# Performance work log

Hardware: AMD Instinct MI355X
Metric: run time of the kernel (lower is better)

## Reference

```python
import jax, jax.numpy as jnp
import numpy as np

B, N, M, E, CD, H, DH, MH = 4, 2048, 512, 512, 256, 8, 64, 1024
EPS = 1e-6

def _ln(x):
    m = x.mean(-1, keepdims=True)
    v = ((x - m) ** 2).mean(-1, keepdims=True)
    return (x - m) / jnp.sqrt(v + EPS)

def _heads(t):  # [B, L, H*DH] -> [B, H, L, DH]
    b, l, _ = t.shape
    return t.reshape(b, l, H, DH).transpose(0, 2, 1, 3)

def _attn(q, k, v, scale):
    sim = jnp.einsum('bhid,bhjd->bhij', q, k) * scale
    a = jax.nn.softmax(sim, axis=-1)
    o = jnp.einsum('bhij,bhjd->bhid', a, v)
    b, h, l, d = o.shape
    return o.transpose(0, 2, 1, 3).reshape(b, l, h * d)

def setup_inputs() -> dict:
    key = jax.random.key(0)
    ks = jax.random.split(key, 16)
    s = 0.02
    return {
        'cond': jax.random.normal(ks[0], (B, M, CD), jnp.float32),
        'x_in': jax.random.normal(ks[1], (B, N, E), jnp.float32),
        # nn.MultiheadAttention params (combined in-proj + out-proj)
        'Wqkv': jax.random.normal(ks[2], (3 * E, E), jnp.float32) * s,
        'b_qkv': jnp.zeros((3 * E,), jnp.float32),
        'Wo': jax.random.normal(ks[3], (E, E), jnp.float32) * s,
        'bo': jnp.zeros((E,), jnp.float32),
        # CrossAttention params (q/k/v no bias, out has bias)
        'Wcq': jax.random.normal(ks[4], (H * DH, E), jnp.float32) * s,
        'Wck': jax.random.normal(ks[5], (H * DH, CD), jnp.float32) * s,
        'Wcv': jax.random.normal(ks[6], (H * DH, CD), jnp.float32) * s,
        'Wco': jax.random.normal(ks[7], (E, H * DH), jnp.float32) * s,
        'bco': jnp.zeros((E,), jnp.float32),
        # MLP params (note: ReLU applied after the LAST layer too, per source)
        'W1': jax.random.normal(ks[8], (MH, E), jnp.float32) * s,
        'b1': jnp.zeros((MH,), jnp.float32),
        'W2': jax.random.normal(ks[9], (E, MH), jnp.float32) * s,
        'b2': jnp.zeros((E,), jnp.float32),
    }

def reference(cond, x_in, Wqkv, b_qkv, Wo, bo, Wcq, Wck, Wcv, Wco, bco, W1, b1, W2, b2):
    # --- self-attention (nn.MultiheadAttention math) ---
    xn = _ln(x_in)
    qkv = xn @ Wqkv.T + b_qkv  # [B,N,3E]
    q, k, v = jnp.split(qkv, 3, axis=-1)
    sa = _attn(_heads(q), _heads(k), _heads(v), 1.0 / jnp.sqrt(jnp.float32(DH)))
    x = sa @ Wo.T + bo + x_in
    # --- cross-attention ---
    xn2 = _ln(x)
    cq = _heads(xn2 @ Wcq.T)
    ck = _heads(cond @ Wck.T)
    cv = _heads(cond @ Wcv.T)
    ca = _attn(cq, ck, cv, DH ** -0.5)
    x = ca @ Wco.T + bco + x
    # --- MLP (ReLU after both layers, as in source) ---
    xn3 = _ln(x)
    h = jax.nn.relu(xn3 @ W1.T + b1)
    m = jax.nn.relu(h @ W2.T + b2)
    return m + x
```

## Files before the change

kernel.cpp:

```cpp
#include <hip/hip_runtime.h>
#include <cstdint>
#include <cstddef>


typedef short short8 __attribute__((ext_vector_type(8)));
typedef short short4v __attribute__((ext_vector_type(4)));
typedef float f32x4 __attribute__((ext_vector_type(4)));
typedef float f32x16 __attribute__((ext_vector_type(16)));

typedef __attribute__((address_space(1))) const void gconst_t;
typedef __attribute__((address_space(3))) void lds_t;

__device__ __forceinline__ void gl_lds16(const void* g, void* l) {
  __builtin_amdgcn_global_load_lds((gconst_t*)g, (lds_t*)l, 16, 0, 0);
}

__device__ __forceinline__ short f2bf(float f) {
  union { float f; unsigned u; } x; x.f = f;
  unsigned r = x.u + 0x7fffu + ((x.u >> 16) & 1u);
  return (short)(r >> 16);
}
__device__ __forceinline__ float bf2f(short s) {
  union { unsigned u; float f; } x; x.u = ((unsigned)(unsigned short)s) << 16;
  return x.f;
}

__device__ __forceinline__ void pl32swap(unsigned& a, unsigned& b) {
  asm("v_permlane32_swap_b32 %0, %1" : "+v"(a), "+v"(b));
}

struct CastDesc { const float* src; short* dst; int nblk; };
struct CastArgs { CastDesc d[9]; };

__global__ __launch_bounds__(256) void cast_multi(CastArgs a) {
  int bi = blockIdx.x;
#pragma unroll
  for (int i = 0; i < 9; ++i) {
    if (bi < a.d[i].nblk) {
      int idx = (bi * 256 + threadIdx.x) * 8;
      const float* src = a.d[i].src;
      float4 f0 = *(const float4*)(src + idx);
      float4 f1 = *(const float4*)(src + idx + 4);
      short8 o;
      o[0] = f2bf(f0.x); o[1] = f2bf(f0.y); o[2] = f2bf(f0.z); o[3] = f2bf(f0.w);
      o[4] = f2bf(f1.x); o[5] = f2bf(f1.y); o[6] = f2bf(f1.z); o[7] = f2bf(f1.w);
      *(short8*)(a.d[i].dst + idx) = o;
      return;
    }
    bi -= a.d[i].nblk;
  }
}

template <bool INBF>
__global__ __launch_bounds__(256) void ln_kernel(
    const void* __restrict__ xin, short* __restrict__ out, int nrows) {
  int row = blockIdx.x * 4 + (threadIdx.x >> 6);
  int lane = threadIdx.x & 63;
  if (row >= nrows) return;
  float v[8];
  if constexpr (INBF) {
    const short* xr = (const short*)xin + (size_t)row * 512 + lane * 8;
    short8 a = *(const short8*)xr;
#pragma unroll
    for (int e = 0; e < 8; ++e) v[e] = bf2f(a[e]);
  } else {
    const float* xr = (const float*)xin + (size_t)row * 512 + lane * 8;
    float4 a = *(const float4*)xr;
    float4 b = *(const float4*)(xr + 4);
    v[0] = a.x; v[1] = a.y; v[2] = a.z; v[3] = a.w;
    v[4] = b.x; v[5] = b.y; v[6] = b.z; v[7] = b.w;
  }
  float s = 0.f;
#pragma unroll
  for (int e = 0; e < 8; ++e) s += v[e];
#pragma unroll
  for (int m = 1; m < 64; m <<= 1) s += __shfl_xor(s, m);
  float mean = s * (1.f / 512.f);
  float sq = 0.f;
#pragma unroll
  for (int e = 0; e < 8; ++e) { float d = v[e] - mean; sq += d * d; }
#pragma unroll
  for (int m = 1; m < 64; m <<= 1) sq += __shfl_xor(sq, m);
  float rstd = rsqrtf(sq * (1.f / 512.f) + 1e-6f);
  short8 o;
#pragma unroll
  for (int e = 0; e < 8; ++e) o[e] = f2bf((v[e] - mean) * rstd);
  *(short8*)(out + (size_t)row * 512 + lane * 8) = o;
}

template <int TN, int RESMODE, bool BIAS, bool RELU, bool OUTBF, bool VT>
__global__ __launch_bounds__(256) void gemm_nt(
    const short* __restrict__ A, const short* __restrict__ W,
    const float* __restrict__ bias, const void* __restrict__ res,
    void* __restrict__ outp, int R, int NC, int K, int gx,
    short* __restrict__ vt, int vcol0, int vn_log2,
    float oscale, int oscale_end) {
  constexpr int NF = TN / 32;
  constexpr int NBUF = (TN == 128) ? 2 : 3;
  __shared__ short As[NBUF][128 * 64];
  __shared__ short Ws[NBUF][TN * 64];
  const int nwg = gridDim.x;
  const int b0 = blockIdx.x;
  const int bid = ((nwg & 7) == 0) ? ((b0 & 7) * (nwg >> 3) + (b0 >> 3)) : b0;
  const int bx = bid % gx, by = bid / gx;
  const int brow = by * 128, bcol = bx * TN;
  const int t = threadIdx.x;
  const int wid = t >> 6, lane = t & 63;
  const int lr = lane & 15, lk = lane >> 4;
  const int wrow = (wid >> 1) * 64, wcol = (wid & 1) * (TN / 2);
  f32x4 acc[4][NF] = {};

  const int srw = lane >> 3;
  const int scol = (((lane & 7) ^ srw) << 3);
  const short* Ag = A + (size_t)(brow + wid * 32 + srw) * K + scol;
  const short* Wg = W + (size_t)(bcol + wid * (TN / 4) + srw) * K + scol;

#define G_STAGE(I, BUF)                                                       \
  {                                                                           \
    const int k0_ = (I) * 64;                                                 \
    gl_lds16(Ag + k0_, &As[BUF][(wid * 32) * 64]);                            \
    gl_lds16(Ag + (size_t)8 * K + k0_, &As[BUF][(wid * 32 + 8) * 64]);        \
    gl_lds16(Ag + (size_t)16 * K + k0_, &As[BUF][(wid * 32 + 16) * 64]);      \
    gl_lds16(Ag + (size_t)24 * K + k0_, &As[BUF][(wid * 32 + 24) * 64]);      \
    if constexpr (TN == 128) {                                                \
      gl_lds16(Wg + k0_, &Ws[BUF][(wid * 32) * 64]);                          \
      gl_lds16(Wg + (size_t)8 * K + k0_, &Ws[BUF][(wid * 32 + 8) * 64]);      \
      gl_lds16(Wg + (size_t)16 * K + k0_, &Ws[BUF][(wid * 32 + 16) * 64]);    \
      gl_lds16(Wg + (size_t)24 * K + k0_, &Ws[BUF][(wid * 32 + 24) * 64]);    \
    } else {                                                                  \
      gl_lds16(Wg + k0_, &Ws[BUF][(wid * 16) * 64]);                          \
      gl_lds16(Wg + (size_t)8 * K + k0_, &Ws[BUF][(wid * 16 + 8) * 64]);      \
    }                                                                         \
  }

  const int ns = K / 64;

#define G_COMPUTE(CUR)                                                        \
  {                                                                           \
    _Pragma("unroll")                                                         \
    for (int kc = 0; kc < 2; ++kc) {                                          \
      short8 af[4], bf[NF];                                                   \
      _Pragma("unroll")                                                       \
      for (int mi = 0; mi < 4; ++mi) {                                        \
        const int row = wrow + mi * 16 + lr;                                  \
        af[mi] = *(const short8*)&As[CUR][row * 64 +                          \
                                          (((kc * 4 + lk) ^ (row & 7)) << 3)];\
      }                                                                       \
      _Pragma("unroll")                                                       \
      for (int ni = 0; ni < NF; ++ni) {                                       \
        const int row = wcol + ni * 16 + lr;                                  \
        bf[ni] = *(const short8*)&Ws[CUR][row * 64 +                          \
                                          (((kc * 4 + lk) ^ (row & 7)) << 3)];\
      }                                                                       \
      _Pragma("unroll")                                                       \
      for (int mi = 0; mi < 4; ++mi)                                          \
        _Pragma("unroll")                                                     \
        for (int ni = 0; ni < NF; ++ni)                                       \
          acc[mi][ni] = __builtin_amdgcn_mfma_f32_16x16x32_bf16(              \
              af[mi], bf[ni], acc[mi][ni], 0, 0, 0);                          \
    }                                                                         \
  }

  if constexpr (TN == 128) {
    G_STAGE(0, 0);
    asm volatile("s_waitcnt vmcnt(0)" ::: "memory");
    __builtin_amdgcn_s_barrier();
    for (int i = 0; i < ns; ++i) {
      const int cur = i & 1;
      if (i + 1 < ns) G_STAGE(i + 1, cur ^ 1);
      G_COMPUTE(cur);
      if (i + 1 < ns) {
        asm volatile("s_waitcnt vmcnt(0) lgkmcnt(0)" ::: "memory");
        __builtin_amdgcn_s_barrier();
      }
    }
  } else {
    G_STAGE(0, 0);
    G_STAGE(1, 1);
    asm volatile("s_waitcnt vmcnt(6)" ::: "memory");
    __builtin_amdgcn_s_barrier();
    for (int i = 0; i < ns; ++i) {
      const int cur = i % 3;
      if (i + 2 < ns) G_STAGE(i + 2, (i + 2) % 3);
      G_COMPUTE(cur);
      if (i + 1 < ns) {
        if (i + 2 < ns)
          asm volatile("s_waitcnt vmcnt(6) lgkmcnt(0)" ::: "memory");
        else
          asm volatile("s_waitcnt vmcnt(0) lgkmcnt(0)" ::: "memory");
        __builtin_amdgcn_s_barrier();
      }
    }
  }
#undef G_STAGE
#undef G_COMPUTE

  if (VT && bcol >= vcol0) {
    const int vn_mask = (1 << vn_log2) - 1;
#pragma unroll
    for (int mi = 0; mi < 4; ++mi) {
#pragma unroll
      for (int ni = 0; ni < NF; ++ni) {
        int col = bcol + wcol + ni * 16 + lr;
        int vc = col - vcol0;
        int r0 = brow + wrow + mi * 16 + lk * 4;
        int bb = r0 >> vn_log2;
        int n = r0 & vn_mask;
        float bv = BIAS ? bias[col] : 0.f;
        short4v o;
#pragma unroll
        for (int j = 0; j < 4; ++j) o[j] = f2bf(acc[mi][ni][j] + bv);
        *(short4v*)(vt + (((size_t)(bb * 512 + vc)) << vn_log2) + n) = o;
      }
    }
    return;
  }

#pragma unroll
  for (int mi = 0; mi < 4; ++mi) {
#pragma unroll
    for (int ni = 0; ni < NF; ++ni) {
      int col = bcol + wcol + ni * 16 + lr;
      int row0 = brow + wrow + mi * 16 + lk * 4;
      float bv = BIAS ? bias[col] : 0.f;
#pragma unroll
      for (int j = 0; j < 4; ++j) {
        float v = acc[mi][ni][j] + bv;
        if (RELU) v = fmaxf(v, 0.f);
        if (col < oscale_end) v *= oscale;
        size_t oi = (size_t)(row0 + j) * NC + col;
        if (RESMODE == 1) v += ((const float*)res)[oi];
        if (RESMODE == 2) v += bf2f(((const short*)res)[oi]);
        if (OUTBF) ((short*)outp)[oi] = f2bf(v);
        else       ((float*)outp)[oi] = v;
      }
    }
  }
}

__global__ __launch_bounds__(256) void flash_attn8(
    const short* __restrict__ q, const short* __restrict__ k,
    const short* __restrict__ vt, short* __restrict__ out,
    int qstride, int kstride, int Nq, int Nkv, int vn_log2, int H_) {
  __shared__ short Ks[2 * 128 * 64];
  __shared__ short Vs[2 * 64 * 128];
  const int t = threadIdx.x;
  const int wid = t >> 6, lane = t & 63;
  const int l31 = lane & 31, lh = lane >> 5;
  const int nb = gridDim.x;
  const int b0 = blockIdx.x;
  const int bid = ((nb & 7) == 0) ? ((b0 & 7) * (nb >> 3) + (b0 >> 3)) : b0;
  const int gx = Nq >> 7;
  const int bh = bid / gx, qblk = bid - bh * gx;
  const int b = bh / H_, h = bh - b * H_;
  const int q0 = qblk * 128 + wid * 32;

  short8 qf[4];
  {
    const short* qp = q + ((size_t)b * Nq + q0 + l31) * qstride + h * 64 + lh * 8;
#pragma unroll
    for (int kc = 0; kc < 4; ++kc) qf[kc] = *(const short8*)(qp + kc * 16);
  }

  f32x16 o0 = {}, o1 = {};
  f32x16 lacc = {};

  const int krw = lane >> 3;
  const short* kG = k + ((size_t)b * Nkv + wid * 32 + krw) * kstride + h * 64 +
                    (((lane & 7) ^ krw) << 3);
  const short* vGp[4];
#pragma unroll
  for (int j = 0; j < 4; ++j)
    vGp[j] = vt + (((size_t)bh * 64 + wid * 16 + j * 4 + (lane >> 4)) << vn_log2) +
             (((lane & 15) ^ (j * 4 + (lane >> 4))) << 3);
  short* kD = &Ks[wid * 2048];
  short* vD = &Vs[wid * 2048];

#define STAGE_KV(KT, BUF)                                                     \
  {                                                                           \
    const short* kp_ = kG + (size_t)(KT) * kstride;                           \
    short* kd_ = kD + (BUF) * 8192;                                           \
    gl_lds16(kp_, kd_);                                                       \
    gl_lds16(kp_ + (size_t)8 * kstride, kd_ + 512);                           \
    gl_lds16(kp_ + (size_t)16 * kstride, kd_ + 1024);                         \
    gl_lds16(kp_ + (size_t)24 * kstride, kd_ + 1536);                         \
    short* vd_ = vD + (BUF) * 8192;                                           \
    gl_lds16(vGp[0] + (KT), vd_);                                             \
    gl_lds16(vGp[1] + (KT), vd_ + 512);                                       \
    gl_lds16(vGp[2] + (KT), vd_ + 1024);                                      \
    gl_lds16(vGp[3] + (KT), vd_ + 1536);                                      \
  }

  STAGE_KV(0, 0);
  __syncthreads();
  int cur = 0;

  for (int kt = 0; kt < Nkv; kt += 128) {
    if (kt + 128 < Nkv) STAGE_KV(kt + 128, cur ^ 1);

    const short* kbase = &Ks[cur * 8192];
    const short* vbase = &Vs[cur * 8192];

#pragma unroll
    for (int kk = 0; kk < 4; ++kk) {
      f32x16 s = {};
      {
        const int r = kk * 32 + l31;
        const short* krow = kbase + r * 64;
        const int rx = r & 7;
#pragma unroll
        for (int kc = 0; kc < 4; ++kc) {
          short8 kf = *(const short8*)(krow + (((kc * 2 + lh) ^ rx) << 3));
          s = __builtin_amdgcn_mfma_f32_32x32x16_bf16(kf, qf[kc], s, 0, 0, 0);
        }
      }
#pragma unroll
      for (int rr = 0; rr < 16; ++rr)
        s[rr] = __builtin_amdgcn_exp2f(s[rr]);
      lacc += s;
      unsigned w[8];
#pragma unroll
      for (int g = 0; g < 8; ++g)
        asm("v_cvt_pk_bf16_f32 %0, %1, %2" : "=v"(w[g]) : "v"(s[2 * g]), "v"(s[2 * g + 1]));
      pl32swap(w[0], w[2]); pl32swap(w[1], w[3]);
      pl32swap(w[4], w[6]); pl32swap(w[5], w[7]);
      union { unsigned u[4]; short8 s8; } pf0, pf1;
      pf0.u[0] = w[0]; pf0.u[1] = w[1]; pf0.u[2] = w[2]; pf0.u[3] = w[3];
      pf1.u[0] = w[4]; pf1.u[1] = w[5]; pf1.u[2] = w[6]; pf1.u[3] = w[7];
#pragma unroll
      for (int ch = 0; ch < 2; ++ch) {
        short8 pf = ch ? pf1.s8 : pf0.s8;
        const int c16 = kk * 4 + ch * 2 + lh;
        {
          const int d = l31;
          short8 vf = *(const short8*)(vbase + d * 128 + ((c16 ^ (d & 15)) << 3));
          o0 = __builtin_amdgcn_mfma_f32_32x32x16_bf16(vf, pf, o0, 0, 0, 0);
        }
        {
          const int d = 32 + l31;
          short8 vf = *(const short8*)(vbase + d * 128 + ((c16 ^ (d & 15)) << 3));
          o1 = __builtin_amdgcn_mfma_f32_32x32x16_bf16(vf, pf, o1, 0, 0, 0);
        }
      }
    }

    __syncthreads();
    cur ^= 1;
  }
#undef STAGE_KV

  float ls = (((lacc[0] + lacc[1]) + (lacc[2] + lacc[3])) +
              ((lacc[4] + lacc[5]) + (lacc[6] + lacc[7]))) +
             (((lacc[8] + lacc[9]) + (lacc[10] + lacc[11])) +
              ((lacc[12] + lacc[13]) + (lacc[14] + lacc[15])));
  ls += __shfl_xor(ls, 32);
  float inv = 1.f / ls;

  short* orow = out + ((size_t)b * Nq + q0 + l31) * 512 + h * 64 + 4 * lh;
#pragma unroll
  for (int g = 0; g < 4; ++g) {
    short4v w0, w1;
#pragma unroll
    for (int j = 0; j < 4; ++j) {
      w0[j] = f2bf(o0[4 * g + j] * inv);
      w1[j] = f2bf(o1[4 * g + j] * inv);
    }
    *(short4v*)(orow + 8 * g) = w0;
    *(short4v*)(orow + 32 + 8 * g) = w1;
  }
}

extern "C" void kernel_launch(void* const* d_in, const int* in_sizes, int n_in,
                              void* d_out, int out_size, void* d_ws, size_t ws_size,
                              hipStream_t stream) {
  (void)in_sizes; (void)n_in; (void)out_size; (void)ws_size;
  const float* cond  = (const float*)d_in[0];
  const float* x_in  = (const float*)d_in[1];
  const float* Wqkv  = (const float*)d_in[2];
  const float* b_qkv = (const float*)d_in[3];
  const float* Wo    = (const float*)d_in[4];
  const float* bo    = (const float*)d_in[5];
  const float* Wcq   = (const float*)d_in[6];
  const float* Wck   = (const float*)d_in[7];
  const float* Wcv   = (const float*)d_in[8];
  const float* Wco   = (const float*)d_in[9];
  const float* bco   = (const float*)d_in[10];
  const float* W1    = (const float*)d_in[11];
  const float* b1    = (const float*)d_in[12];
  const float* W2    = (const float*)d_in[13];
  const float* b2    = (const float*)d_in[14];
  float* out = (float*)d_out;

  const int Bv = 4, Nv = 2048, Mv = 512, Ev = 512, Hv = 8, MHv = 1024, CDv = 256;
  const int RN = Bv * Nv;
  const int RM = Bv * Mv;
  const float KSC = 0.125f * 1.44269504f;

  char* ws = (char*)d_ws;
  size_t off = 0;
  auto alloc = [&](size_t bytes) { void* p = ws + off; off += bytes; return p; };

  short* wqkv_b = (short*)alloc((size_t)3 * Ev * Ev * 2);
  short* wo_b   = (short*)alloc((size_t)Ev * Ev * 2);
  short* wcq_b  = (short*)alloc((size_t)Ev * Ev * 2);
  short* wck_b  = (short*)alloc((size_t)Ev * CDv * 2);
  short* wcv_b  = (short*)alloc((size_t)Ev * CDv * 2);
  short* wco_b  = (short*)alloc((size_t)Ev * Ev * 2);
  short* w1_b   = (short*)alloc((size_t)MHv * Ev * 2);
  short* w2_b   = (short*)alloc((size_t)Ev * MHv * 2);
  short* cond_b = (short*)alloc((size_t)RM * CDv * 2);
  short* xnb    = (short*)alloc((size_t)RN * Ev * 2);
  short* sa_b   = (short*)alloc((size_t)RN * Ev * 2);
  short* x1     = (short*)alloc((size_t)RN * Ev * 2);
  short* x2     = (short*)alloc((size_t)RN * Ev * 2);
  char*  qreg   = (char*)alloc((size_t)RN * 3 * Ev * 2);
  short* qkv_b  = (short*)qreg;
  short* cq   = (short*)(qreg + 0);
  short* ck   = (short*)(qreg + (size_t)RN * Ev * 2);
  short* vt_c = (short*)(qreg + (size_t)RN * Ev * 2 + (size_t)4 * 1024 * 1024);
  short* ca   = (short*)(qreg + (size_t)RN * Ev * 2 + (size_t)6 * 1024 * 1024);
  short* hb   = (short*)(qreg + 0);
  short* vt_s = (short*)x2;

  CastArgs ca_args;
  const float* srcs[9] = {Wqkv, Wo, Wcq, Wck, Wcv, Wco, W1, W2, cond};
  short* dsts[9] = {wqkv_b, wo_b, wcq_b, wck_b, wcv_b, wco_b, w1_b, w2_b, cond_b};
  int ns_[9] = {3*Ev*Ev, Ev*Ev, Ev*Ev, Ev*CDv, Ev*CDv, Ev*Ev, MHv*Ev, Ev*MHv, RM*CDv};
  int tot_blk = 0;
  for (int i = 0; i < 9; ++i) {
    ca_args.d[i].src = srcs[i]; ca_args.d[i].dst = dsts[i];
    ca_args.d[i].nblk = ns_[i] / 2048; tot_blk += ca_args.d[i].nblk;
  }
  cast_multi<<<tot_blk, 256, 0, stream>>>(ca_args);

  dim3 blk(256);

  ln_kernel<false><<<RN / 4, blk, 0, stream>>>(x_in, xnb, RN);
  gemm_nt<128, 0, true, false, true, true><<<(3 * Ev / 128) * (RN / 128), blk, 0, stream>>>(
      xnb, wqkv_b, b_qkv, nullptr, qkv_b, RN, 3 * Ev, Ev, 3 * Ev / 128,
      vt_s, 2 * Ev, 11, KSC, Ev);
  flash_attn8<<<(Nv / 128) * Bv * Hv, blk, 0, stream>>>(
      qkv_b, qkv_b + Ev, vt_s, sa_b, 3 * Ev, 3 * Ev, Nv, Nv, 11, Hv);
  gemm_nt<64, 1, true, false, true, false><<<(Ev / 64) * (RN / 128), blk, 0, stream>>>(
      sa_b, wo_b, bo, x_in, x1, RN, Ev, Ev, Ev / 64, nullptr, 0, 0, 1.f, 0);
  ln_kernel<true><<<RN / 4, blk, 0, stream>>>(x1, xnb, RN);
  gemm_nt<64, 0, false, false, true, false><<<(Ev / 64) * (RN / 128), blk, 0, stream>>>(
      xnb, wcq_b, nullptr, nullptr, cq, RN, Ev, Ev, Ev / 64, nullptr, 0, 0, KSC, Ev);
  gemm_nt<64, 0, false, false, true, true><<<(2 * Ev / 64) * (RM / 128), blk, 0, stream>>>(
      cond_b, wck_b, nullptr, nullptr, ck, RM, 2 * Ev, CDv, 2 * Ev / 64,
      vt_c, Ev, 9, 1.f, 0);
  flash_attn8<<<(Nv / 128) * Bv * Hv, blk, 0, stream>>>(
      cq, ck, vt_c, ca, Ev, 2 * Ev, Nv, Mv, 9, Hv);
  gemm_nt<64, 2, true, false, true, false><<<(Ev / 64) * (RN / 128), blk, 0, stream>>>(
      ca, wco_b, bco, x1, x2, RN, Ev, Ev, Ev / 64, nullptr, 0, 0, 1.f, 0);
  ln_kernel<true><<<RN / 4, blk, 0, stream>>>(x2, xnb, RN);
  gemm_nt<128, 0, true, true, true, false><<<(MHv / 128) * (RN / 128), blk, 0, stream>>>(
      xnb, w1_b, b1, nullptr, hb, RN, MHv, Ev, MHv / 128, nullptr, 0, 0, 1.f, 0);
  gemm_nt<64, 2, true, true, false, false><<<(Ev / 64) * (RN / 128), blk, 0, stream>>>(
      hb, w2_b, b2, x2, out, RN, Ev, MHv, Ev / 64, nullptr, 0, 0, 1.f, 0);
}
```

Measured before the change: 189.0 us.

## Swap MFMA operands for vectorized GEMM epilogues and batch attention QK/PV phases

Adds a SWAPC GEMM variant that passes the MFMA operands in swapped order. Each lane then holds four consecutive output columns of one row, so bias, residual and output go through vector loads and stores instead of strided scalar accesses. The attention kernel is restructured to compute all four QK score tiles first, then exp and pack them, then run all PV MFMAs. The MFMA phases are wrapped in s_setprio to improve matrix-core issue overlap across waves. The cost is higher register pressure from holding four score accumulators and the packed P fragments, which could reduce occupancy.

Result: slower. 193.6 us (+2.5%).

```diff
diff --git a/kernel.cpp b/kernel.cpp
--- a/kernel.cpp
+++ b/kernel.cpp
@@ -88,7 +88,7 @@
   *(short8*)(out + (size_t)row * 512 + lane * 8) = o;
 }
 
-template <int TN, int RESMODE, bool BIAS, bool RELU, bool OUTBF, bool VT>
+template <int TN, int RESMODE, bool BIAS, bool RELU, bool OUTBF, bool VT, bool SWAPC>
 __global__ __launch_bounds__(256) void gemm_nt(
     const short* __restrict__ A, const short* __restrict__ W,
     const float* __restrict__ bias, const void* __restrict__ res,
@@ -155,9 +155,14 @@
       _Pragma("unroll")                                                       \
       for (int mi = 0; mi < 4; ++mi)                                          \
         _Pragma("unroll")                                                     \
-        for (int ni = 0; ni < NF; ++ni)                                       \
-          acc[mi][ni] = __builtin_amdgcn_mfma_f32_16x16x32_bf16(              \
-              af[mi], bf[ni], acc[mi][ni], 0, 0, 0);                          \
+        for (int ni = 0; ni < NF; ++ni) {                                     \
+          if constexpr (SWAPC)                                                \
+            acc[mi][ni] = __builtin_amdgcn_mfma_f32_16x16x32_bf16(            \
+                bf[ni], af[mi], acc[mi][ni], 0, 0, 0);                        \
+          else                                                                \
+            acc[mi][ni] = __builtin_amdgcn_mfma_f32_16x16x32_bf16(            \
+                af[mi], bf[ni], acc[mi][ni], 0, 0, 0);                        \
+        }                                                                     \
     }                                                                         \
   }
 
@@ -195,6 +200,48 @@
 #undef G_STAGE
 #undef G_COMPUTE
 
+  if constexpr (SWAPC) {
+#pragma unroll
+    for (int mi = 0; mi < 4; ++mi) {
+#pragma unroll
+      for (int ni = 0; ni < NF; ++ni) {
+        const int row = brow + wrow + mi * 16 + lr;
+        const int colb = bcol + wcol + ni * 16 + lk * 4;
+        f32x4 v = acc[mi][ni];
+        if (BIAS) {
+          float4 bv = *(const float4*)&bias[colb];
+          v[0] += bv.x; v[1] += bv.y; v[2] += bv.z; v[3] += bv.w;
+        }
+        if (RELU) {
+#pragma unroll
+          for (int j = 0; j < 4; ++j) v[j] = fmaxf(v[j], 0.f);
+        }
+        if (colb < oscale_end) {
+#pragma unroll
+          for (int j = 0; j < 4; ++j) v[j] *= oscale;
+        }
+        size_t oi = (size_t)row * NC + colb;
+        if (RESMODE == 1) {
+          float4 r = *(const float4*)((const float*)res + oi);
+          v[0] += r.x; v[1] += r.y; v[2] += r.z; v[3] += r.w;
+        } else if (RESMODE == 2) {
+          short4v r = *(const short4v*)((const short*)res + oi);
+#pragma unroll
+          for (int j = 0; j < 4; ++j) v[j] += bf2f(r[j]);
+        }
+        if (OUTBF) {
+          short4v o;
+#pragma unroll
+          for (int j = 0; j < 4; ++j) o[j] = f2bf(v[j]);
+          *(short4v*)((short*)outp + oi) = o;
+        } else {
+          *(f32x4*)((float*)outp + oi) = v;
+        }
+      }
+    }
+    return;
+  }
+
   if (VT && bcol >= vcol0) {
     const int vn_mask = (1 << vn_log2) - 1;
 #pragma unroll
@@ -238,7 +285,7 @@
   }
 }
 
-__global__ __launch_bounds__(256) void flash_attn8(
+__global__ __launch_bounds__(256) void flash_attn9(
     const short* __restrict__ q, const short* __restrict__ k,
     const short* __restrict__ vt, short* __restrict__ out,
     int qstride, int kstride, int Nq, int Nkv, int vn_log2, int H_) {
@@ -301,48 +348,61 @@
     const short* kbase = &Ks[cur * 8192];
     const short* vbase = &Vs[cur * 8192];
 
+    f32x16 s[4] = {};
+    __builtin_amdgcn_s_setprio(1);
 #pragma unroll
     for (int kk = 0; kk < 4; ++kk) {
-      f32x16 s = {};
-      {
-        const int r = kk * 32 + l31;
-        const short* krow = kbase + r * 64;
-        const int rx = r & 7;
-#pragma unroll
-        for (int kc = 0; kc < 4; ++kc) {
-          short8 kf = *(const short8*)(krow + (((kc * 2 + lh) ^ rx) << 3));
-          s = __builtin_amdgcn_mfma_f32_32x32x16_bf16(kf, qf[kc], s, 0, 0, 0);
-        }
-      }
+      const int r = kk * 32 + l31;
+      const short* krow = kbase + r * 64;
+      const int rx = r & 7;
+#pragma unroll
+      for (int kc = 0; kc < 4; ++kc) {
+        short8 kf = *(const short8*)(krow + (((kc * 2 + lh) ^ rx) << 3));
+        s[kk] = __builtin_amdgcn_mfma_f32_32x32x16_bf16(kf, qf[kc], s[kk], 0, 0, 0);
+      }
+    }
+    __builtin_amdgcn_s_setprio(0);
+
+    short8 pf[4][2];
+#pragma unroll
+    for (int kk = 0; kk < 4; ++kk) {
 #pragma unroll
       for (int rr = 0; rr < 16; ++rr)
-        s[rr] = __builtin_amdgcn_exp2f(s[rr]);
-      lacc += s;
+        s[kk][rr] = __builtin_amdgcn_exp2f(s[kk][rr]);
+      lacc += s[kk];
       unsigned w[8];
 #pragma unroll
       for (int g = 0; g < 8; ++g)
-        asm("v_cvt_pk_bf16_f32 %0, %1, %2" : "=v"(w[g]) : "v"(s[2 * g]), "v"(s[2 * g + 1]));
+        asm("v_cvt_pk_bf16_f32 %0, %1, %2"
+            : "=v"(w[g]) : "v"(s[kk][2 * g]), "v"(s[kk][2 * g + 1]));
       pl32swap(w[0], w[2]); pl32swap(w[1], w[3]);
       pl32swap(w[4], w[6]); pl32swap(w[5], w[7]);
-      union { unsigned u[4]; short8 s8; } pf0, pf1;
-      pf0.u[0] = w[0]; pf0.u[1] = w[1]; pf0.u[2] = w[2]; pf0.u[3] = w[3];
-      pf1.u[0] = w[4]; pf1.u[1] = w[5]; pf1.u[2] = w[6]; pf1.u[3] = w[7];
+      union { unsigned u[4]; short8 s8; } u0, u1;
+      u0.u[0] = w[0]; u0.u[1] = w[1]; u0.u[2] = w[2]; u0.u[3] = w[3];
+      u1.u[0] = w[4]; u1.u[1] = w[5]; u1.u[2] = w[6]; u1.u[3] = w[7];
+      pf[kk][0] = u0.s8;
+      pf[kk][1] = u1.s8;
+    }
+
+    __builtin_amdgcn_s_setprio(1);
+#pragma unroll
+    for (int kk = 0; kk < 4; ++kk) {
 #pragma unroll
       for (int ch = 0; ch < 2; ++ch) {
-        short8 pf = ch ? pf1.s8 : pf0.s8;
         const int c16 = kk * 4 + ch * 2 + lh;
         {
           const int d = l31;
           short8 vf = *(const short8*)(vbase + d * 128 + ((c16 ^ (d & 15)) << 3));
-          o0 = __builtin_amdgcn_mfma_f32_32x32x16_bf16(vf, pf, o0, 0, 0, 0);
+          o0 = __builtin_amdgcn_mfma_f32_32x32x16_bf16(vf, pf[kk][ch], o0, 0, 0, 0);
         }
         {
           const int d = 32 + l31;
           short8 vf = *(const short8*)(vbase + d * 128 + ((c16 ^ (d & 15)) << 3));
-          o1 = __builtin_amdgcn_mfma_f32_32x32x16_bf16(vf, pf, o1, 0, 0, 0);
-        }
-      }
-    }
+          o1 = __builtin_amdgcn_mfma_f32_32x32x16_bf16(vf, pf[kk][ch], o1, 0, 0, 0);
+        }
+      }
+    }
+    __builtin_amdgcn_s_setprio(0);
 
     __syncthreads();
     cur ^= 1;
@@ -436,26 +496,26 @@
   dim3 blk(256);
 
   ln_kernel<false><<<RN / 4, blk, 0, stream>>>(x_in, xnb, RN);
-  gemm_nt<128, 0, true, false, true, true><<<(3 * Ev / 128) * (RN / 128), blk, 0, stream>>>(
+  gemm_nt<128, 0, true, false, true, true, false><<<(3 * Ev / 128) * (RN / 128), blk, 0, stream>>>(
       xnb, wqkv_b, b_qkv, nullptr, qkv_b, RN, 3 * Ev, Ev, 3 * Ev / 128,
       vt_s, 2 * Ev, 11, KSC, Ev);
-  flash_attn8<<<(Nv / 128) * Bv * Hv, blk, 0, stream>>>(
+  flash_attn9<<<(Nv / 128) * Bv * Hv, blk, 0, stream>>>(
       qkv_b, qkv_b + Ev, vt_s, sa_b, 3 * Ev, 3 * Ev, Nv, Nv, 11, Hv);
-  gemm_nt<64, 1, true, false, true, false><<<(Ev / 64) * (RN / 128), blk, 0, stream>>>(
+  gemm_nt<64, 1, true, false, true, false, true><<<(Ev / 64) * (RN / 128), blk, 0, stream>>>(
       sa_b, wo_b, bo, x_in, x1, RN, Ev, Ev, Ev / 64, nullptr, 0, 0, 1.f, 0);
   ln_kernel<true><<<RN / 4, blk, 0, stream>>>(x1, xnb, RN);
-  gemm_nt<64, 0, false, false, true, false><<<(Ev / 64) * (RN / 128), blk, 0, stream>>>(
+  gemm_nt<64, 0, false, false, true, false, true><<<(Ev / 64) * (RN / 128), blk, 0, stream>>>(
       xnb, wcq_b, nullptr, nullptr, cq, RN, Ev, Ev, Ev / 64, nullptr, 0, 0, KSC, Ev);
-  gemm_nt<64, 0, false, false, true, true><<<(2 * Ev / 64) * (RM / 128), blk, 0, stream>>>(
+  gemm_nt<64, 0, false, false, true, true, false><<<(2 * Ev / 64) * (RM / 128), blk, 0, stream>>>(
       cond_b, wck_b, nullptr, nullptr, ck, RM, 2 * Ev, CDv, 2 * Ev / 64,
       vt_c, Ev, 9, 1.f, 0);
-  flash_attn8<<<(Nv / 128) * Bv * Hv, blk, 0, stream>>>(
+  flash_attn9<<<(Nv / 128) * Bv * Hv, blk, 0, stream>>>(
       cq, ck, vt_c, ca, Ev, 2 * Ev, Nv, Mv, 9, Hv);
-  gemm_nt<64, 2, true, false, true, false><<<(Ev / 64) * (RN / 128), blk, 0, stream>>>(
+  gemm_nt<64, 2, true, false, true, false, true><<<(Ev / 64) * (RN / 128), blk, 0, stream>>>(
       ca, wco_b, bco, x1, x2, RN, Ev, Ev, Ev / 64, nullptr, 0, 0, 1.f, 0);
   ln_kernel<true><<<RN / 4, blk, 0, stream>>>(x2, xnb, RN);
-  gemm_nt<128, 0, true, true, true, false><<<(MHv / 128) * (RN / 128), blk, 0, stream>>>(
+  gemm_nt<128, 0, true, true, true, false, true><<<(MHv / 128) * (RN / 128), blk, 0, stream>>>(
       xnb, w1_b, b1, nullptr, hb, RN, MHv, Ev, MHv / 128, nullptr, 0, 0, 1.f, 0);
-  gemm_nt<64, 2, true, true, false, false><<<(Ev / 64) * (RN / 128), blk, 0, stream>>>(
+  gemm_nt<64, 2, true, true, false, false, true><<<(Ev / 64) * (RN / 128), blk, 0, stream>>>(
       hb, w2_b, b2, x2, out, RN, Ev, MHv, Ev / 64, nullptr, 0, 0, 1.f, 0);
 }
```

## Split self-attention KV range in two and merge partial outputs

Applied to the files above, without the earlier changes.

Self-attention now runs as a split-KV flash kernel: each query block handles half of the key/value sequence, writes unnormalised bf16 partial outputs and row sums, and a new merge kernel adds the two halves and normalises. This doubles the grid (512 to 1024 blocks) to improve occupancy and load balance across CUs. In exchange it adds an extra kernel launch plus about 8 MB of partial-output traffic, and rounds the unnormalised partials to bf16. Like the original, it relies on no max subtraction (exp2 of raw scores).

Result: slower. 200.8 us (+6.3%).

```diff
diff --git a/kernel.cpp b/kernel.cpp
--- a/kernel.cpp
+++ b/kernel.cpp
@@ -370,6 +370,152 @@
   }
 }
 
+__global__ __launch_bounds__(256) void flash_attn10(
+    const short* __restrict__ q, const short* __restrict__ k,
+    const short* __restrict__ vt, short* __restrict__ opart,
+    float* __restrict__ lpart,
+    int qstride, int kstride, int Nq, int Nkv, int vn_log2, int H_) {
+  __shared__ short Ks[2 * 64 * 64];
+  __shared__ short Vs[2 * 64 * 64];
+  const int t = threadIdx.x;
+  const int wid = t >> 6, lane = t & 63;
+  const int l31 = lane & 31, lh = lane >> 5;
+  const int nb = gridDim.x;
+  const int b0 = blockIdx.x;
+  const int bid = ((nb & 7) == 0) ? ((b0 & 7) * (nb >> 3) + (b0 >> 3)) : b0;
+  const int split = bid & 1;
+  const int rest = bid >> 1;
+  const int gx = Nq >> 7;
+  const int bh = rest / gx, qblk = rest - bh * gx;
+  const int b = bh / H_, h = bh - b * H_;
+  const int q0 = qblk * 128 + wid * 32;
+  const int kvlen = Nkv >> 1;
+  const int kt0 = split * kvlen;
+
+  short8 qf[4];
+  {
+    const short* qp = q + ((size_t)b * Nq + q0 + l31) * qstride + h * 64 + lh * 8;
+#pragma unroll
+    for (int kc = 0; kc < 4; ++kc) qf[kc] = *(const short8*)(qp + kc * 16);
+  }
+
+  f32x16 o0 = {}, o1 = {};
+  f32x16 lacc = {};
+
+  const int srw8 = lane >> 3;
+  const int scb = ((lane & 7) ^ srw8) << 3;
+  const short* kG = k + ((size_t)b * Nkv + wid * 16 + srw8) * kstride + h * 64 + scb;
+  const short* vG = vt + (((size_t)bh * 64 + wid * 16 + srw8) << vn_log2) + scb;
+  short* kD = &Ks[wid * 1024];
+  short* vD = &Vs[wid * 1024];
+
+#define STAGE_KV64(KT, BUF)                                                   \
+  {                                                                           \
+    const short* kp_ = kG + (size_t)(KT) * kstride;                           \
+    gl_lds16(kp_, kD + (BUF) * 4096);                                         \
+    gl_lds16(kp_ + (size_t)8 * kstride, kD + (BUF) * 4096 + 512);             \
+    const short* vp_ = vG + (KT);                                             \
+    gl_lds16(vp_, vD + (BUF) * 4096);                                         \
+    gl_lds16(vp_ + ((size_t)8 << vn_log2), vD + (BUF) * 4096 + 512);          \
+  }
+
+  STAGE_KV64(kt0, 0);
+  __syncthreads();
+  int cur = 0;
+
+  for (int kt = kt0; kt < kt0 + kvlen; kt += 64) {
+    if (kt + 64 < kt0 + kvlen) STAGE_KV64(kt + 64, cur ^ 1);
+
+    const short* kbase = &Ks[cur * 4096];
+    const short* vbase = &Vs[cur * 4096];
+
+#pragma unroll
+    for (int kk = 0; kk < 2; ++kk) {
+      f32x16 s = {};
+      {
+        const int r = kk * 32 + l31;
+        const short* krow = kbase + r * 64;
+        const int rx = r & 7;
+#pragma unroll
+        for (int kc = 0; kc < 4; ++kc) {
+          short8 kf = *(const short8*)(krow + (((kc * 2 + lh) ^ rx) << 3));
+          s = __builtin_amdgcn_mfma_f32_32x32x16_bf16(kf, qf[kc], s, 0, 0, 0);
+        }
+      }
+#pragma unroll
+      for (int rr = 0; rr < 16; ++rr)
+        s[rr] = __builtin_amdgcn_exp2f(s[rr]);
+      lacc += s;
+      unsigned w[8];
+#pragma unroll
+      for (int g = 0; g < 8; ++g)
+        asm("v_cvt_pk_bf16_f32 %0, %1, %2" : "=v"(w[g]) : "v"(s[2 * g]), "v"(s[2 * g + 1]));
+      pl32swap(w[0], w[2]); pl32swap(w[1], w[3]);
+      pl32swap(w[4], w[6]); pl32swap(w[5], w[7]);
+      union { unsigned u[4]; short8 s8; } pf0, pf1;
+      pf0.u[0] = w[0]; pf0.u[1] = w[1]; pf0.u[2] = w[2]; pf0.u[3] = w[3];
+      pf1.u[0] = w[4]; pf1.u[1] = w[5]; pf1.u[2] = w[6]; pf1.u[3] = w[7];
+#pragma unroll
+      for (int ch = 0; ch < 2; ++ch) {
+        short8 pf = ch ? pf1.s8 : pf0.s8;
+        const int c8 = kk * 4 + ch * 2 + lh;
+        {
+          const int d = l31;
+          short8 vf = *(const short8*)(vbase + d * 64 + ((c8 ^ (d & 7)) << 3));
+          o0 = __builtin_amdgcn_mfma_f32_32x32x16_bf16(vf, pf, o0, 0, 0, 0);
+        }
+        {
+          const int d = 32 + l31;
+          short8 vf = *(const short8*)(vbase + d * 64 + ((c8 ^ (d & 7)) << 3));
+          o1 = __builtin_amdgcn_mfma_f32_32x32x16_bf16(vf, pf, o1, 0, 0, 0);
+        }
+      }
+    }
+
+    __syncthreads();
+    cur ^= 1;
+  }
+#undef STAGE_KV64
+
+  float ls = (((lacc[0] + lacc[1]) + (lacc[2] + lacc[3])) +
+              ((lacc[4] + lacc[5]) + (lacc[6] + lacc[7]))) +
+             (((lacc[8] + lacc[9]) + (lacc[10] + lacc[11])) +
+              ((lacc[12] + lacc[13]) + (lacc[14] + lacc[15])));
+  ls += __shfl_xor(ls, 32);
+
+  const size_t prow = ((size_t)(split * 32 + bh) * Nq + q0 + l31);
+  short* orow = opart + prow * 64 + 4 * lh;
+#pragma unroll
+  for (int g = 0; g < 4; ++g) {
+    short4v w0, w1;
+#pragma unroll
+    for (int j = 0; j < 4; ++j) {
+      w0[j] = f2bf(o0[4 * g + j]);
+      w1[j] = f2bf(o1[4 * g + j]);
+    }
+    *(short4v*)(orow + 8 * g) = w0;
+    *(short4v*)(orow + 32 + 8 * g) = w1;
+  }
+  if (lh == 0) lpart[prow] = ls;
+}
+
+__global__ __launch_bounds__(256) void merge_attn(
+    const short* __restrict__ oP, const float* __restrict__ lP,
+    short* __restrict__ out, int Nq, int H_, int BHN) {
+  const int t = threadIdx.x;
+  const int R = blockIdx.x * 32 + (t >> 3);
+  const int d0 = (t & 7) * 8;
+  const int bh = R / Nq, qq = R - bh * Nq;
+  const int b = bh / H_, h = bh - b * H_;
+  short8 a = *(const short8*)(oP + (size_t)R * 64 + d0);
+  short8 c = *(const short8*)(oP + ((size_t)BHN + R) * 64 + d0);
+  float inv = 1.f / (lP[R] + lP[BHN + R]);
+  short8 o;
+#pragma unroll
+  for (int j = 0; j < 8; ++j) o[j] = f2bf((bf2f(a[j]) + bf2f(c[j])) * inv);
+  *(short8*)(out + ((size_t)(b * Nq + qq)) * 512 + h * 64 + d0) = o;
+}
+
 extern "C" void kernel_launch(void* const* d_in, const int* in_sizes, int n_in,
                               void* d_out, int out_size, void* d_ws, size_t ws_size,
                               hipStream_t stream) {
@@ -394,6 +540,7 @@
   const int Bv = 4, Nv = 2048, Mv = 512, Ev = 512, Hv = 8, MHv = 1024, CDv = 256;
   const int RN = Bv * Nv;
   const int RM = Bv * Mv;
+  const int BHN = Bv * Hv * Nv;
   const float KSC = 0.125f * 1.44269504f;
 
   char* ws = (char*)d_ws;
@@ -413,6 +560,8 @@
   short* sa_b   = (short*)alloc((size_t)RN * Ev * 2);
   short* x1     = (short*)alloc((size_t)RN * Ev * 2);
   short* x2     = (short*)alloc((size_t)RN * Ev * 2);
+  short* oP     = (short*)alloc((size_t)2 * BHN * 64 * 2);
+  float* lP     = (float*)alloc((size_t)2 * BHN * 4);
   char*  qreg   = (char*)alloc((size_t)RN * 3 * Ev * 2);
   short* qkv_b  = (short*)qreg;
   short* cq   = (short*)(qreg + 0);
@@ -439,8 +588,9 @@
   gemm_nt<128, 0, true, false, true, true><<<(3 * Ev / 128) * (RN / 128), blk, 0, stream>>>(
       xnb, wqkv_b, b_qkv, nullptr, qkv_b, RN, 3 * Ev, Ev, 3 * Ev / 128,
       vt_s, 2 * Ev, 11, KSC, Ev);
-  flash_attn8<<<(Nv / 128) * Bv * Hv, blk, 0, stream>>>(
-      qkv_b, qkv_b + Ev, vt_s, sa_b, 3 * Ev, 3 * Ev, Nv, Nv, 11, Hv);
+  flash_attn10<<<(Nv / 128) * Bv * Hv * 2, blk, 0, stream>>>(
+      qkv_b, qkv_b + Ev, vt_s, oP, lP, 3 * Ev, 3 * Ev, Nv, Nv, 11, Hv);
+  merge_attn<<<BHN / 32, blk, 0, stream>>>(oP, lP, sa_b, Nv, Hv, BHN);
   gemm_nt<64, 1, true, false, true, false><<<(Ev / 64) * (RN / 128), blk, 0, stream>>>(
       sa_b, wo_b, bo, x_in, x1, RN, Ev, Ev, Ev / 64, nullptr, 0, 0, 1.f, 0);
   ln_kernel<true><<<RN / 4, blk, 0, stream>>>(x1, xnb, RN);
```
